# Performance work log

Measured on AMD Instinct MI355X. Metric: run time of the kernel, lower is better.

## Reference

```python
import jax, jax.numpy as jnp
import numpy as np

EPS = 1e-4

def setup_inputs() -> dict:
    key = jax.random.key(0)
    k1, k2, k3 = jax.random.split(key, 3)
    B, IN, OUT = 8192, 4096, 4096
    x = jax.random.normal(k1, (B, IN), dtype=jnp.float32)
    # torch Linear default init: U(-1/sqrt(in), 1/sqrt(in)); scale randn similarly
    scale = 1.0 / np.sqrt(IN)
    W = jax.random.uniform(k2, (OUT, IN), dtype=jnp.float32, minval=-scale, maxval=scale)
    b = jax.random.uniform(k3, (OUT,), dtype=jnp.float32, minval=-scale, maxval=scale)
    return {"x": x, "W": W, "b": b}

def reference(x, W, b):
    # row-wise L2 normalize (with +1e-4 in denominator, matching torch code)
    norm = jnp.sqrt(jnp.sum(x * x, axis=1, keepdims=True))
    x_dir = x / (norm + EPS)
    # linear: y = x_dir @ W^T + b, then ReLU
    y = jnp.einsum('bi,oi->bo', x_dir, W) + b
    return jax.nn.relu(y)
```

## Files before the change

### kernel.cpp

```cpp
#include <hip/hip_runtime.h>
#include <hip/hip_bf16.h>
#include <stdint.h>
#include <stddef.h>

typedef int i32x4 __attribute__((ext_vector_type(4)));

#define B_DIM 8192
#define K_DIM 4096
#define N_DIM 4096

typedef __attribute__((address_space(1))) const void gvoid_t;
typedef __attribute__((address_space(3))) void lvoid_t;

__device__ __forceinline__ void gload_lds16(const void* g, void* l) {
  __builtin_amdgcn_global_load_lds((gvoid_t*)g, (lvoid_t*)l, 16, 0, 0);
}

#define FENCE() asm volatile("" ::: "memory")
#define BARRIER() do { FENCE(); __builtin_amdgcn_s_barrier(); FENCE(); } while (0)

__device__ __forceinline__ int q8(float v, float inv) {
  float f = v * inv;
  f = fminf(fmaxf(f, -127.f), 127.f);
  return __float2int_rn(f) & 0xff;
}

__global__ __launch_bounds__(256) void prep_kernel(
    const float* __restrict__ x, const float* __restrict__ W,
    int8_t* __restrict__ xq, int8_t* __restrict__ wq,
    float* __restrict__ sa, float* __restrict__ sw) {
  const int t = threadIdx.x;
  const int lane = t & 63, wv = t >> 6;
  __shared__ float wsum[4], wamax[4];
  __shared__ float s_inv, s_scale;

  if (blockIdx.x < B_DIM) {
    const int row = blockIdx.x;
    const float4* xr = (const float4*)(x + (size_t)row * K_DIM);
    float4 v[4];
    float ss = 0.f, am = 0.f;
#pragma unroll
    for (int i = 0; i < 4; ++i) {
      v[i] = xr[i * 256 + t];
      ss += v[i].x * v[i].x + v[i].y * v[i].y + v[i].z * v[i].z + v[i].w * v[i].w;
      am = fmaxf(am, fmaxf(fmaxf(fabsf(v[i].x), fabsf(v[i].y)),
                           fmaxf(fabsf(v[i].z), fabsf(v[i].w))));
    }
#pragma unroll
    for (int o = 32; o > 0; o >>= 1) {
      ss += __shfl_down(ss, o, 64);
      am = fmaxf(am, __shfl_down(am, o, 64));
    }
    if (lane == 0) { wsum[wv] = ss; wamax[wv] = am; }
    __syncthreads();
    if (t == 0) {
      float s = wsum[0] + wsum[1] + wsum[2] + wsum[3];
      float a = fmaxf(fmaxf(wamax[0], wamax[1]), fmaxf(wamax[2], wamax[3]));
      a = fmaxf(a, 1e-20f);
      float sc = 1.0f / (sqrtf(s) + 1e-4f);
      s_inv = 127.0f / a;
      s_scale = a * sc / 127.0f;
      sa[row] = s_scale;
    }
    __syncthreads();
    const float inv = s_inv;
    uint32_t* orow = (uint32_t*)(xq + (size_t)row * K_DIM);
#pragma unroll
    for (int i = 0; i < 4; ++i) {
      uint32_t p = (uint32_t)q8(v[i].x, inv) | ((uint32_t)q8(v[i].y, inv) << 8) |
                   ((uint32_t)q8(v[i].z, inv) << 16) | ((uint32_t)q8(v[i].w, inv) << 24);
      orow[i * 256 + t] = p;
    }
  } else {
    const int row = blockIdx.x - B_DIM;
    const float4* wr = (const float4*)(W + (size_t)row * K_DIM);
    float4 v[4];
    float am = 0.f;
#pragma unroll
    for (int i = 0; i < 4; ++i) {
      v[i] = wr[i * 256 + t];
      am = fmaxf(am, fmaxf(fmaxf(fabsf(v[i].x), fabsf(v[i].y)),
                           fmaxf(fabsf(v[i].z), fabsf(v[i].w))));
    }
#pragma unroll
    for (int o = 32; o > 0; o >>= 1) am = fmaxf(am, __shfl_down(am, o, 64));
    if (lane == 0) wamax[wv] = am;
    __syncthreads();
    if (t == 0) {
      float a = fmaxf(fmaxf(wamax[0], wamax[1]), fmaxf(wamax[2], wamax[3]));
      a = fmaxf(a, 1e-20f);
      s_inv = 127.0f / a;
      sw[row] = a / 127.0f;
    }
    __syncthreads();
    const float inv = s_inv;
    uint32_t* orow = (uint32_t*)(wq + (size_t)row * K_DIM);
#pragma unroll
    for (int i = 0; i < 4; ++i) {
      uint32_t p = (uint32_t)q8(v[i].x, inv) | ((uint32_t)q8(v[i].y, inv) << 8) |
                   ((uint32_t)q8(v[i].z, inv) << 16) | ((uint32_t)q8(v[i].w, inv) << 24);
      orow[i * 256 + t] = p;
    }
  }
}

__global__ __launch_bounds__(512, 1) void gemm_kernel(
    const int8_t* __restrict__ A, const int8_t* __restrict__ Bm,
    const float* __restrict__ sa, const float* __restrict__ sw,
    const float* __restrict__ bias, float* __restrict__ C) {
  __shared__ __align__(16) char lds[131072];
  const int tid = threadIdx.x;
  const int lane = tid & 63, w = tid >> 6;
  const int wm = w >> 2, wn = w & 3;
  const int hi16 = lane >> 4;
  const int r16 = lane & 15;

  const int bid = blockIdx.x;
  const int sid = (bid & 7) * 64 + (bid >> 3);
  const int mb = sid & 31;
  const int nb = sid >> 5;

  const char* Ag = (const char*)A + (size_t)mb * 256 * K_DIM;
  const char* Bg = (const char*)Bm + (size_t)nb * 256 * K_DIM;

  auto STAGE = [&](int mat, int h, int kt) {
    const int rbase = (kt & 1) * 65536 + mat * 32768 + h * 16384;
    const char* gb = (mat == 0 ? Ag : Bg) + (size_t)h * 128 * K_DIM + kt * 128;
#pragma unroll
    for (int i = 0; i < 2; ++i) {
      const int qb = i * 8192 + w * 1024;
      const int q = qb + lane * 16;
      const int r = q >> 7;
      const int cb = (q & 127) ^ ((r & 7) << 4);
      gload_lds16(gb + (size_t)r * K_DIM + cb, lds + rbase + qb);
    }
  };
  auto LDA = [&](int m, int kq, int cur) -> i32x4 {
    const int r = m * 16 + r16;
    const int q = (r << 7) + (kq << 6) + hi16 * 16;
    return *(const i32x4*)(lds + cur * 65536 + wm * 16384 + (q ^ ((r & 7) << 4)));
  };
  auto LDB = [&](int n, int kq, int cur) -> i32x4 {
    const int r = (wn & 1) * 64 + n * 16 + r16;
    const int q = (r << 7) + (kq << 6) + hi16 * 16;
    return *(const i32x4*)(lds + cur * 65536 + 32768 + (wn >> 1) * 16384 + (q ^ ((r & 7) << 4)));
  };

  i32x4 acc[8][4] = {};
  i32x4 af[4][2], bfr[4][2];

  STAGE(0, 0, 0); STAGE(0, 1, 0); STAGE(1, 0, 0); STAGE(1, 1, 0);
  STAGE(1, 0, 1); STAGE(1, 1, 1);
  asm volatile("s_waitcnt vmcnt(4)" ::: "memory");
  BARRIER();

  for (int u = 0; u < 32; ++u) {
    const int cur = u & 1;
    const int un1 = (u + 1) & 31, un2 = (u + 2) & 31;
#pragma unroll
    for (int m = 0; m < 4; ++m)
#pragma unroll
      for (int kq = 0; kq < 2; ++kq) af[m][kq] = LDA(m, kq, cur);
#pragma unroll
    for (int n = 0; n < 2; ++n)
#pragma unroll
      for (int kq = 0; kq < 2; ++kq) bfr[n][kq] = LDB(n, kq, cur);
    STAGE(0, 0, un1);
    BARRIER();
    __builtin_amdgcn_s_setprio(1);
#pragma unroll
    for (int kq = 0; kq < 2; ++kq)
#pragma unroll
      for (int m = 0; m < 4; ++m)
#pragma unroll
        for (int n = 0; n < 2; ++n)
          acc[m][n] = __builtin_amdgcn_mfma_i32_16x16x64_i8(af[m][kq], bfr[n][kq], acc[m][n], 0, 0, 0);
    __builtin_amdgcn_s_setprio(0);
    BARRIER();
#pragma unroll
    for (int n = 2; n < 4; ++n)
#pragma unroll
      for (int kq = 0; kq < 2; ++kq) bfr[n][kq] = LDB(n, kq, cur);
    STAGE(0, 1, un1);
    BARRIER();
    __builtin_amdgcn_s_setprio(1);
#pragma unroll
    for (int kq = 0; kq < 2; ++kq)
#pragma unroll
      for (int m = 0; m < 4; ++m)
#pragma unroll
        for (int n = 2; n < 4; ++n)
          acc[m][n] = __builtin_amdgcn_mfma_i32_16x16x64_i8(af[m][kq], bfr[n][kq], acc[m][n], 0, 0, 0);
    __builtin_amdgcn_s_setprio(0);
    BARRIER();
#pragma unroll
    for (int m = 0; m < 4; ++m)
#pragma unroll
      for (int kq = 0; kq < 2; ++kq) af[m][kq] = LDA(m + 4, kq, cur);
    STAGE(1, 0, un2);
    BARRIER();
    __builtin_amdgcn_s_setprio(1);
#pragma unroll
    for (int kq = 0; kq < 2; ++kq)
#pragma unroll
      for (int m = 0; m < 4; ++m)
#pragma unroll
        for (int n = 0; n < 2; ++n)
          acc[m + 4][n] = __builtin_amdgcn_mfma_i32_16x16x64_i8(af[m][kq], bfr[n][kq], acc[m + 4][n], 0, 0, 0);
    __builtin_amdgcn_s_setprio(0);
    BARRIER();
    STAGE(1, 1, un2);
    BARRIER();
    __builtin_amdgcn_s_setprio(1);
#pragma unroll
    for (int kq = 0; kq < 2; ++kq)
#pragma unroll
      for (int m = 0; m < 4; ++m)
#pragma unroll
        for (int n = 2; n < 4; ++n)
          acc[m + 4][n] = __builtin_amdgcn_mfma_i32_16x16x64_i8(af[m][kq], bfr[n][kq], acc[m + 4][n], 0, 0, 0);
    __builtin_amdgcn_s_setprio(0);
    asm volatile("s_waitcnt vmcnt(4)" ::: "memory");
    BARRIER();
  }

  float bv[4], sbn[4];
#pragma unroll
  for (int n = 0; n < 4; ++n) {
    const int col = nb * 256 + wn * 64 + n * 16 + r16;
    bv[n] = bias[col];
    sbn[n] = sw[col];
  }
#pragma unroll
  for (int m = 0; m < 8; ++m) {
    const int row0 = mb * 256 + wm * 128 + m * 16 + hi16 * 4;
#pragma unroll
    for (int j = 0; j < 4; ++j) {
      const float sv = sa[row0 + j];
      float* crow = C + (size_t)(row0 + j) * N_DIM + nb * 256 + wn * 64 + r16;
#pragma unroll
      for (int n = 0; n < 4; ++n)
        crow[n * 16] = fmaxf((float)acc[m][n][j] * (sv * sbn[n]) + bv[n], 0.f);
    }
  }
}

extern "C" void kernel_launch(void* const* d_in, const int* in_sizes, int n_in,
                              void* d_out, int out_size, void* d_ws, size_t ws_size,
                              hipStream_t stream) {
  const float* x = (const float*)d_in[0];
  const float* W = (const float*)d_in[1];
  const float* b = (const float*)d_in[2];
  float* out = (float*)d_out;

  int8_t* xq = (int8_t*)d_ws;
  int8_t* wq = xq + (size_t)B_DIM * K_DIM;
  float* sa = (float*)(wq + (size_t)N_DIM * K_DIM);
  float* sw = sa + B_DIM;

  prep_kernel<<<B_DIM + N_DIM, 256, 0, stream>>>(x, W, xq, wq, sa, sw);
  gemm_kernel<<<32 * 16, 512, 0, stream>>>(xq, wq, sa, sw, b, out);
}
```

Measured before the change: 197.3 us.

## Shrink GEMM tile to 128x128 with 256 threads and two blocks per CU

The int8 GEMM moves from 256x256 tiles with 512 threads and 128KB of LDS to 128x128 tiles with 256 threads, 64KB of LDS and two blocks per CU. The per-iteration schedule drops from four MFMA phases to two, and all B fragments are loaded up front. This gives more blocks (2048 instead of 512) and lets two blocks share a CU to hide latency. The cost is half the data reuse per tile, so global and L2 traffic roughly doubles.

```diff
diff --git a/kernel.cpp b/kernel.cpp
--- a/kernel.cpp
+++ b/kernel.cpp
@@ -32,7 +32,7 @@
   const int t = threadIdx.x;
   const int lane = t & 63, wv = t >> 6;
   __shared__ float wsum[4], wamax[4];
-  __shared__ float s_inv, s_scale;
+  __shared__ float s_inv;
 
   if (blockIdx.x < B_DIM) {
     const int row = blockIdx.x;
@@ -59,8 +59,7 @@
       a = fmaxf(a, 1e-20f);
       float sc = 1.0f / (sqrtf(s) + 1e-4f);
       s_inv = 127.0f / a;
-      s_scale = a * sc / 127.0f;
-      sa[row] = s_scale;
+      sa[row] = a * sc / 127.0f;
     }
     __syncthreads();
     const float inv = s_inv;
@@ -104,31 +103,31 @@
   }
 }
 
-__global__ __launch_bounds__(512, 1) void gemm_kernel(
+__global__ __launch_bounds__(256, 2) void gemm_kernel(
     const int8_t* __restrict__ A, const int8_t* __restrict__ Bm,
     const float* __restrict__ sa, const float* __restrict__ sw,
     const float* __restrict__ bias, float* __restrict__ C) {
-  __shared__ __align__(16) char lds[131072];
+  __shared__ __align__(16) char lds[65536];
   const int tid = threadIdx.x;
   const int lane = tid & 63, w = tid >> 6;
-  const int wm = w >> 2, wn = w & 3;
+  const int wm = w >> 1, wn = w & 1;
   const int hi16 = lane >> 4;
   const int r16 = lane & 15;
 
   const int bid = blockIdx.x;
-  const int sid = (bid & 7) * 64 + (bid >> 3);
-  const int mb = sid & 31;
-  const int nb = sid >> 5;
-
-  const char* Ag = (const char*)A + (size_t)mb * 256 * K_DIM;
-  const char* Bg = (const char*)Bm + (size_t)nb * 256 * K_DIM;
+  const int sid = (bid & 7) * 256 + (bid >> 3);
+  const int mb = sid & 63;
+  const int nb = sid >> 6;
+
+  const char* Ag = (const char*)A + (size_t)mb * 128 * K_DIM;
+  const char* Bg = (const char*)Bm + (size_t)nb * 128 * K_DIM;
 
   auto STAGE = [&](int mat, int h, int kt) {
-    const int rbase = (kt & 1) * 65536 + mat * 32768 + h * 16384;
-    const char* gb = (mat == 0 ? Ag : Bg) + (size_t)h * 128 * K_DIM + kt * 128;
+    const int rbase = (kt & 1) * 32768 + mat * 16384 + h * 8192;
+    const char* gb = (mat == 0 ? Ag : Bg) + (size_t)h * 64 * K_DIM + kt * 128;
 #pragma unroll
     for (int i = 0; i < 2; ++i) {
-      const int qb = i * 8192 + w * 1024;
+      const int qb = i * 4096 + w * 1024;
       const int q = qb + lane * 16;
       const int r = q >> 7;
       const int cb = (q & 127) ^ ((r & 7) << 4);
@@ -136,17 +135,17 @@
     }
   };
   auto LDA = [&](int m, int kq, int cur) -> i32x4 {
-    const int r = m * 16 + r16;
+    const int r = wm * 64 + m * 16 + r16;
     const int q = (r << 7) + (kq << 6) + hi16 * 16;
-    return *(const i32x4*)(lds + cur * 65536 + wm * 16384 + (q ^ ((r & 7) << 4)));
+    return *(const i32x4*)(lds + cur * 32768 + (q ^ ((r & 7) << 4)));
   };
   auto LDB = [&](int n, int kq, int cur) -> i32x4 {
-    const int r = (wn & 1) * 64 + n * 16 + r16;
+    const int r = wn * 64 + n * 16 + r16;
     const int q = (r << 7) + (kq << 6) + hi16 * 16;
-    return *(const i32x4*)(lds + cur * 65536 + 32768 + (wn >> 1) * 16384 + (q ^ ((r & 7) << 4)));
+    return *(const i32x4*)(lds + cur * 32768 + 16384 + (q ^ ((r & 7) << 4)));
   };
 
-  i32x4 acc[8][4] = {};
+  i32x4 acc[4][4] = {};
   i32x4 af[4][2], bfr[4][2];
 
   STAGE(0, 0, 0); STAGE(0, 1, 0); STAGE(1, 0, 0); STAGE(1, 1, 0);
@@ -162,10 +161,11 @@
 #pragma unroll
       for (int kq = 0; kq < 2; ++kq) af[m][kq] = LDA(m, kq, cur);
 #pragma unroll
-    for (int n = 0; n < 2; ++n)
+    for (int n = 0; n < 4; ++n)
 #pragma unroll
       for (int kq = 0; kq < 2; ++kq) bfr[n][kq] = LDB(n, kq, cur);
     STAGE(0, 0, un1);
+    STAGE(0, 1, un1);
     BARRIER();
     __builtin_amdgcn_s_setprio(1);
 #pragma unroll
@@ -177,11 +177,8 @@
           acc[m][n] = __builtin_amdgcn_mfma_i32_16x16x64_i8(af[m][kq], bfr[n][kq], acc[m][n], 0, 0, 0);
     __builtin_amdgcn_s_setprio(0);
     BARRIER();
-#pragma unroll
-    for (int n = 2; n < 4; ++n)
-#pragma unroll
-      for (int kq = 0; kq < 2; ++kq) bfr[n][kq] = LDB(n, kq, cur);
-    STAGE(0, 1, un1);
+    STAGE(1, 0, un2);
+    STAGE(1, 1, un2);
     BARRIER();
     __builtin_amdgcn_s_setprio(1);
 #pragma unroll
@@ -192,34 +189,6 @@
         for (int n = 2; n < 4; ++n)
           acc[m][n] = __builtin_amdgcn_mfma_i32_16x16x64_i8(af[m][kq], bfr[n][kq], acc[m][n], 0, 0, 0);
     __builtin_amdgcn_s_setprio(0);
-    BARRIER();
-#pragma unroll
-    for (int m = 0; m < 4; ++m)
-#pragma unroll
-      for (int kq = 0; kq < 2; ++kq) af[m][kq] = LDA(m + 4, kq, cur);
-    STAGE(1, 0, un2);
-    BARRIER();
-    __builtin_amdgcn_s_setprio(1);
-#pragma unroll
-    for (int kq = 0; kq < 2; ++kq)
-#pragma unroll
-      for (int m = 0; m < 4; ++m)
-#pragma unroll
-        for (int n = 0; n < 2; ++n)
-          acc[m + 4][n] = __builtin_amdgcn_mfma_i32_16x16x64_i8(af[m][kq], bfr[n][kq], acc[m + 4][n], 0, 0, 0);
-    __builtin_amdgcn_s_setprio(0);
-    BARRIER();
-    STAGE(1, 1, un2);
-    BARRIER();
-    __builtin_amdgcn_s_setprio(1);
-#pragma unroll
-    for (int kq = 0; kq < 2; ++kq)
-#pragma unroll
-      for (int m = 0; m < 4; ++m)
-#pragma unroll
-        for (int n = 2; n < 4; ++n)
-          acc[m + 4][n] = __builtin_amdgcn_mfma_i32_16x16x64_i8(af[m][kq], bfr[n][kq], acc[m + 4][n], 0, 0, 0);
-    __builtin_amdgcn_s_setprio(0);
     asm volatile("s_waitcnt vmcnt(4)" ::: "memory");
     BARRIER();
   }
@@ -227,17 +196,17 @@
   float bv[4], sbn[4];
 #pragma unroll
   for (int n = 0; n < 4; ++n) {
-    const int col = nb * 256 + wn * 64 + n * 16 + r16;
+    const int col = nb * 128 + wn * 64 + n * 16 + r16;
     bv[n] = bias[col];
     sbn[n] = sw[col];
   }
 #pragma unroll
-  for (int m = 0; m < 8; ++m) {
-    const int row0 = mb * 256 + wm * 128 + m * 16 + hi16 * 4;
+  for (int m = 0; m < 4; ++m) {
+    const int row0 = mb * 128 + wm * 64 + m * 16 + hi16 * 4;
 #pragma unroll
     for (int j = 0; j < 4; ++j) {
       const float sv = sa[row0 + j];
-      float* crow = C + (size_t)(row0 + j) * N_DIM + nb * 256 + wn * 64 + r16;
+      float* crow = C + (size_t)(row0 + j) * N_DIM + nb * 128 + wn * 64 + r16;
 #pragma unroll
       for (int n = 0; n < 4; ++n)
         crow[n * 16] = fmaxf((float)acc[m][n][j] * (sv * sbn[n]) + bv[n], 0.f);
@@ -259,5 +228,5 @@
   float* sw = sa + B_DIM;
 
   prep_kernel<<<B_DIM + N_DIM, 256, 0, stream>>>(x, W, xq, wq, sa, sw);
-  gemm_kernel<<<32 * 16, 512, 0, stream>>>(xq, wq, sa, sw, b, out);
-}
+  gemm_kernel<<<64 * 32, 256, 0, stream>>>(xq, wq, sa, sw, b, out);
+}
```

New measurement: 224.8 us. +13.9%, slower.
